# Kernel optimization log

Measured on AMD Instinct MI355X. Metric: run time of the kernel, lower is better.

The kernel has to match this reference:

```python
import jax, jax.numpy as jnp
import numpy as np

B = 16
H = W = 56
C = 384
WS = 7            # window size
SS = 3            # shift size
NH = 12           # num heads
HD = C // NH      # head dim
N = WS * WS       # tokens per window (49)
NW = (H // WS) * (W // WS)  # windows per image (64)
HID = 4 * C       # MLP hidden
SCALE = HD ** -0.5
EPS = 1e-5


def _rel_pos_index():
    coords = np.stack(np.meshgrid(np.arange(WS), np.arange(WS), indexing='ij')).reshape(2, -1)
    rel = (coords[:, :, None] - coords[:, None, :]).transpose(1, 2, 0)  # [N,N,2]
    rel[:, :, 0] += WS - 1
    rel[:, :, 1] += WS - 1
    rel[:, :, 0] *= 2 * WS - 1
    return rel.sum(-1).astype(np.int32)  # [N,N] in [0, (2WS-1)^2)


def _attn_mask():
    img = np.zeros((H, W))
    cnt = 0
    for hs in (slice(0, -WS), slice(-WS, -SS), slice(-SS, None)):
        for ws in (slice(0, -WS), slice(-WS, -SS), slice(-SS, None)):
            img[hs, ws] = cnt
            cnt += 1
    mw = img.reshape(H // WS, WS, W // WS, WS).transpose(0, 2, 1, 3).reshape(-1, N)  # [NW,N]
    d = mw[:, None, :] - mw[:, :, None]  # [NW,N,N]
    return np.where(d != 0, -100.0, 0.0).astype(np.float32)


def setup_inputs() -> dict:
    key = jax.random.key(0)
    ks = jax.random.split(key, 8)
    std = 0.02
    return {
        'x': jax.random.normal(ks[0], (B, H * W, C), jnp.float32),
        'g1': jnp.ones((C,), jnp.float32),
        'b1': jnp.zeros((C,), jnp.float32),
        'qkv_w': jax.random.normal(ks[1], (C, 3 * C), jnp.float32) * std,
        'qkv_b': jnp.zeros((3 * C,), jnp.float32),
        'rpb_table': jax.random.normal(ks[2], ((2 * WS - 1) ** 2, NH), jnp.float32) * std,
        'proj_w': jax.random.normal(ks[3], (C, C), jnp.float32) * std,
        'proj_b': jnp.zeros((C,), jnp.float32),
        'g2': jnp.ones((C,), jnp.float32),
        'b2': jnp.zeros((C,), jnp.float32),
        'fc1_w': jax.random.normal(ks[4], (C, HID), jnp.float32) * std,
        'fc1_b': jnp.zeros((HID,), jnp.float32),
        'fc2_w': jax.random.normal(ks[5], (HID, C), jnp.float32) * std,
        'fc2_b': jnp.zeros((C,), jnp.float32),
        'rel_idx': jnp.asarray(_rel_pos_index()),
        'attn_mask': jnp.asarray(_attn_mask()),
    }


def _ln(x, g, b):
    m = x.mean(-1, keepdims=True)
    v = ((x - m) ** 2).mean(-1, keepdims=True)
    return (x - m) / jnp.sqrt(v + EPS) * g + b


def reference(x, g1, b1, qkv_w, qkv_b, rpb_table, proj_w, proj_b,
              g2, b2, fc1_w, fc1_b, fc2_w, fc2_b, rel_idx, attn_mask):
    shortcut = x
    h = _ln(x, g1, b1).reshape(B, H, W, C)
    # cyclic shift
    h = jnp.roll(h, (-SS, -SS), axis=(1, 2))
    # window partition -> [B*NW, N, C]
    win = h.reshape(B, H // WS, WS, W // WS, WS, C).transpose(0, 1, 3, 2, 4, 5).reshape(-1, N, C)
    # qkv
    qkv = (win @ qkv_w + qkv_b).reshape(-1, N, 3, NH, HD).transpose(2, 0, 3, 1, 4)
    q, k, v = qkv[0] * SCALE, qkv[1], qkv[2]  # [B*NW, NH, N, HD]
    attn = jnp.einsum('bhnd,bhmd->bhnm', q, k)  # [B*NW, NH, N, N]
    # relative position bias
    rpb = rpb_table[rel_idx.reshape(-1)].reshape(N, N, NH).transpose(2, 0, 1)  # [NH,N,N]
    attn = attn + rpb[None]
    # shifted-window attention mask
    attn = attn.reshape(B, NW, NH, N, N) + attn_mask[None, :, None]
    attn = jax.nn.softmax(attn.reshape(-1, NH, N, N), axis=-1)
    out = jnp.einsum('bhnm,bhmd->bhnd', attn, v).transpose(0, 2, 1, 3).reshape(-1, N, C)
    out = out @ proj_w + proj_b
    # window reverse + reverse shift
    out = out.reshape(B, H // WS, W // WS, WS, WS, C).transpose(0, 1, 3, 2, 4, 5).reshape(B, H, W, C)
    out = jnp.roll(out, (SS, SS), axis=(1, 2)).reshape(B, H * W, C)
    x = shortcut + out
    # MLP (exact GELU, as nn.GELU default)
    h2 = _ln(x, g2, b2)
    h2 = jax.nn.gelu(h2 @ fc1_w + fc1_b, approximate=False) @ fc2_w + fc2_b
    return x + h2
```

## Files before the change

### kernel.cpp

```cpp
#include <hip/hip_runtime.h>
#include <hip/hip_bf16.h>
#include <math.h>

typedef __hip_bfloat16 bf16;
typedef __attribute__((ext_vector_type(8))) short short8;
typedef __attribute__((ext_vector_type(4))) float f32x4;

#define C_DIM 384
#define SS 3
#define SCALE_ATTN 0.17677669529663687f
#define LN_EPS 1e-5f

typedef const __attribute__((address_space(1))) void g_cvoid;
typedef __attribute__((address_space(3))) void l_void;
__device__ __forceinline__ void gl_lds16(const void* g, void* l) {
    __builtin_amdgcn_global_load_lds((g_cvoid*)g, (l_void*)l, 16, 0, 0);
}

__global__ void transpose_cast_kernel(const float* __restrict__ in, bf16* __restrict__ out,
                                      int R, int Cc) {
    int idx = blockIdx.x * 256 + threadIdx.x;
    if (idx < R * Cc) {
        int r = idx / Cc, c = idx - r * Cc;
        out[(size_t)c * R + r] = __float2bfloat16(in[idx]);
    }
}

__global__ void build_bm_kernel(const float* __restrict__ rpb, const int* __restrict__ rel_idx,
                                const float* __restrict__ mask, float* __restrict__ BM) {
    int idx = blockIdx.x * 256 + threadIdx.x;
    int col = idx & 63, row = (idx >> 6) & 63;
    int h = (idx >> 12) % 12, wi = idx / (12 * 4096);
    float v = -1e30f;
    if (row < 49 && col < 49)
        v = rpb[rel_idx[row * 49 + col] * 12 + h] + mask[(size_t)wi * 2401 + row * 49 + col];
    BM[idx] = v;
}

__global__ __launch_bounds__(256)
void ln1_shift_window(const float* __restrict__ x, const float* __restrict__ g,
                      const float* __restrict__ bta, bf16* __restrict__ win) {
    int wave = threadIdx.x >> 6, lane = threadIdx.x & 63;
    int token = blockIdx.x * 4 + wave;
    int bw = token / 49, ntk = token - bw * 49;
    int bb = bw >> 6, wi = bw & 63;
    int wh = wi >> 3, wwi = wi & 7;
    int rr = ntk / 7, cc = ntk - rr * 7;
    int hs = wh * 7 + rr + SS; if (hs >= 56) hs -= 56;
    int ws = wwi * 7 + cc + SS; if (ws >= 56) ws -= 56;
    const float* src = x + ((size_t)(bb * 3136 + hs * 56 + ws)) * C_DIM;

    float v[6]; float s = 0.f, sq = 0.f;
    #pragma unroll
    for (int j = 0; j < 6; j++) {
        v[j] = src[lane + j * 64];
        s += v[j]; sq += v[j] * v[j];
    }
    #pragma unroll
    for (int o = 32; o > 0; o >>= 1) { s += __shfl_xor(s, o, 64); sq += __shfl_xor(sq, o, 64); }
    float mean = s * (1.0f / 384.0f);
    float var  = sq * (1.0f / 384.0f) - mean * mean;
    float rstd = rsqrtf(var + LN_EPS);

    bf16* dst = win + (size_t)token * C_DIM;
    #pragma unroll
    for (int j = 0; j < 6; j++) {
        int c = lane + j * 64;
        dst[c] = __float2bfloat16((v[j] - mean) * rstd * g[c] + bta[c]);
    }
}

__global__ __launch_bounds__(256)
void ln2_kernel(const float* __restrict__ xmid, const float* __restrict__ g,
                const float* __restrict__ bta, bf16* __restrict__ out) {
    int wave = threadIdx.x >> 6, lane = threadIdx.x & 63;
    int token = blockIdx.x * 4 + wave;
    const float* src = xmid + (size_t)token * C_DIM;
    float v[6]; float s = 0.f, sq = 0.f;
    #pragma unroll
    for (int j = 0; j < 6; j++) {
        v[j] = src[lane + j * 64];
        s += v[j]; sq += v[j] * v[j];
    }
    #pragma unroll
    for (int o = 32; o > 0; o >>= 1) { s += __shfl_xor(s, o, 64); sq += __shfl_xor(sq, o, 64); }
    float mean = s * (1.0f / 384.0f);
    float var  = sq * (1.0f / 384.0f) - mean * mean;
    float rstd = rsqrtf(var + LN_EPS);
    bf16* dst = out + (size_t)token * C_DIM;
    #pragma unroll
    for (int j = 0; j < 6; j++) {
        int c = lane + j * 64;
        dst[c] = __float2bfloat16((v[j] - mean) * rstd * g[c] + bta[c]);
    }
}

template <int MODE>
__global__ __launch_bounds__(256)
void gemm_kernel(const bf16* __restrict__ A, const bf16* __restrict__ BT,
                 const float* __restrict__ bias, void* __restrict__ out,
                 const float* __restrict__ resid, int M, int N, int K) {
    __shared__ bf16 As[8192];
    __shared__ bf16 Bs[8192];

    int tid = threadIdx.x;
    int wave = tid >> 6, lane = tid & 63, quad = lane >> 4, r = lane & 15;
    int wave_m = wave & 1, wave_n = wave >> 1;
    int m0 = blockIdx.x * 128, n0 = blockIdx.y * 128;

    f32x4 acc[4][4] = {};

    for (int k0 = 0; k0 < K; k0 += 64) {
        #pragma unroll
        for (int c = 0; c < 4; c++) {
            int slot = c * 256 + wave * 64 + lane;
            int panel = slot >> 7, row = slot & 127;
            gl_lds16(A + (size_t)(m0 + row) * K + k0 + panel * 8, &As[(c * 256 + wave * 64) * 8]);
            gl_lds16(BT + (size_t)(n0 + row) * K + k0 + panel * 8, &Bs[(c * 256 + wave * 64) * 8]);
        }
        __syncthreads();

        #pragma unroll
        for (int ks = 0; ks < 2; ks++) {
            int pq = ks * 4 + quad;
            short8 a[4], b[4];
            #pragma unroll
            for (int mt = 0; mt < 4; mt++)
                a[mt] = *(const short8*)&As[(pq * 128 + wave_m * 64 + mt * 16 + r) * 8];
            #pragma unroll
            for (int nt = 0; nt < 4; nt++)
                b[nt] = *(const short8*)&Bs[(pq * 128 + wave_n * 64 + nt * 16 + r) * 8];
            #pragma unroll
            for (int mt = 0; mt < 4; mt++)
                #pragma unroll
                for (int nt = 0; nt < 4; nt++)
                    acc[mt][nt] = __builtin_amdgcn_mfma_f32_16x16x32_bf16(
                        a[mt], b[nt], acc[mt][nt], 0, 0, 0);
        }
        __syncthreads();
    }

    #pragma unroll
    for (int mt = 0; mt < 4; mt++) {
        #pragma unroll
        for (int nt = 0; nt < 4; nt++) {
            int n = n0 + wave_n * 64 + nt * 16 + r;
            float bv = bias[n];
            #pragma unroll
            for (int reg = 0; reg < 4; reg++) {
                int m = m0 + wave_m * 64 + mt * 16 + quad * 4 + reg;
                float v = acc[mt][nt][reg] + bv;
                if (MODE == 0) {
                    ((bf16*)out)[(size_t)m * N + n] = __float2bfloat16(v);
                } else if (MODE == 1) {
                    float gl = 0.5f * v * (1.0f + erff(v * 0.70710678118654752f));
                    ((bf16*)out)[(size_t)m * N + n] = __float2bfloat16(gl);
                } else if (MODE == 2) {
                    int bw = m / 49, ntk = m - bw * 49;
                    int bb = bw >> 6, wi = bw & 63;
                    int wh = wi >> 3, wwi = wi & 7;
                    int rr = ntk / 7, cc = ntk - rr * 7;
                    int ho = wh * 7 + rr + SS; if (ho >= 56) ho -= 56;
                    int wo = wwi * 7 + cc + SS; if (wo >= 56) wo -= 56;
                    size_t dst = ((size_t)(bb * 3136 + ho * 56 + wo)) * C_DIM + n;
                    ((float*)out)[dst] = v + resid[dst];
                } else {
                    size_t idx = (size_t)m * N + n;
                    ((float*)out)[idx] = v + resid[idx];
                }
            }
        }
    }
}

__global__ __launch_bounds__(256)
void attn_mfma_kernel(const bf16* __restrict__ qkv, const float* __restrict__ BM,
                      bf16* __restrict__ out) {
    __shared__ bf16 P_lds[4][4096];
    __shared__ bf16 V_lds[4][2048];
    int wave = threadIdx.x >> 6, lane = threadIdx.x & 63;
    int quad = lane >> 4, m16 = lane & 15;
    int bw = blockIdx.x;
    int h = blockIdx.y * 4 + wave;
    int wi = bw & 63;

    const bf16* base = qkv + (size_t)bw * 49 * 1152 + h * 32;

    bf16* Vt = V_lds[wave];
    #pragma unroll
    for (int it = 0; it < 16; it++) {
        int idx = it * 64 + lane;
        int n = idx >> 4, dp = idx & 15;
        int d0 = dp * 2;
        unsigned val = 0;
        if (n < 49)
            val = *(const unsigned*)(base + (size_t)n * 1152 + 768 + d0);
        bf16 v0 = ((const bf16*)&val)[0], v1 = ((const bf16*)&val)[1];
        int cb = (n & 56);
        Vt[d0 * 64 + ((cb ^ ((d0 & 7) << 3)) | (n & 7))] = v0;
        int d1 = d0 + 1;
        Vt[d1 * 64 + ((cb ^ ((d1 & 7) << 3)) | (n & 7))] = v1;
    }

    short8 qf[4], kf[4];
    #pragma unroll
    for (int t = 0; t < 4; t++) {
        int row = t * 16 + m16;
        int rc = (row < 49) ? row : 0;
        qf[t] = *(const short8*)(base + (size_t)rc * 1152 + quad * 8);
        kf[t] = *(const short8*)(base + (size_t)rc * 1152 + 384 + quad * 8);
    }
    f32x4 S[4][4] = {};
    #pragma unroll
    for (int mt = 0; mt < 4; mt++)
        #pragma unroll
        for (int nt = 0; nt < 4; nt++)
            S[mt][nt] = __builtin_amdgcn_mfma_f32_16x16x32_bf16(qf[mt], kf[nt], S[mt][nt], 0, 0, 0);

    const float* bmw = BM + (((size_t)wi * 12 + h) << 12);
    bf16* Pw = P_lds[wave];
    #pragma unroll
    for (int mt = 0; mt < 4; mt++) {
        #pragma unroll
        for (int reg = 0; reg < 4; reg++) {
            int row = mt * 16 + quad * 4 + reg;
            float p[4];
            float mx = -1e30f;
            #pragma unroll
            for (int nt = 0; nt < 4; nt++) {
                int col = nt * 16 + m16;
                float s = S[mt][nt][reg] * SCALE_ATTN + bmw[row * 64 + col];
                p[nt] = s;
                mx = fmaxf(mx, s);
            }
            #pragma unroll
            for (int o = 1; o < 16; o <<= 1) mx = fmaxf(mx, __shfl_xor(mx, o, 64));
            float sm = 0.f;
            #pragma unroll
            for (int nt = 0; nt < 4; nt++) { p[nt] = __expf(p[nt] - mx); sm += p[nt]; }
            #pragma unroll
            for (int o = 1; o < 16; o <<= 1) sm += __shfl_xor(sm, o, 64);
            float inv = 1.0f / sm;
            int r7 = (row & 7) << 3;
            #pragma unroll
            for (int nt = 0; nt < 4; nt++) {
                int col = nt * 16 + m16;
                int sw = ((col & 56) ^ r7) | (col & 7);
                Pw[row * 64 + sw] = __float2bfloat16(p[nt] * inv);
            }
        }
    }

    f32x4 O[4][2] = {};
    #pragma unroll
    for (int ks = 0; ks < 2; ks++) {
        int chunk = ks * 4 + quad;
        short8 pa[4], vb[2];
        #pragma unroll
        for (int mt = 0; mt < 4; mt++) {
            int row = mt * 16 + m16;
            pa[mt] = *(const short8*)&Pw[row * 64 + ((chunk ^ (row & 7)) << 3)];
        }
        #pragma unroll
        for (int nt = 0; nt < 2; nt++) {
            int d = nt * 16 + m16;
            vb[nt] = *(const short8*)&Vt[d * 64 + ((chunk ^ (d & 7)) << 3)];
        }
        #pragma unroll
        for (int mt = 0; mt < 4; mt++)
            #pragma unroll
            for (int nt = 0; nt < 2; nt++)
                O[mt][nt] = __builtin_amdgcn_mfma_f32_16x16x32_bf16(pa[mt], vb[nt], O[mt][nt], 0, 0, 0);
    }

    bf16* orow = out + (size_t)bw * 49 * 384 + h * 32;
    #pragma unroll
    for (int mt = 0; mt < 4; mt++) {
        #pragma unroll
        for (int reg = 0; reg < 4; reg++) {
            int row = mt * 16 + quad * 4 + reg;
            if (row < 49) {
                #pragma unroll
                for (int nt = 0; nt < 2; nt++)
                    orow[(size_t)row * 384 + nt * 16 + m16] = __float2bfloat16(O[mt][nt][reg]);
            }
        }
    }
}

extern "C" void kernel_launch(void* const* d_in, const int* in_sizes, int n_in,
                              void* d_out, int out_size, void* d_ws, size_t ws_size,
                              hipStream_t stream) {
    const float* x      = (const float*)d_in[0];
    const float* g1     = (const float*)d_in[1];
    const float* b1     = (const float*)d_in[2];
    const float* qkv_w  = (const float*)d_in[3];
    const float* qkv_b  = (const float*)d_in[4];
    const float* rpb    = (const float*)d_in[5];
    const float* proj_w = (const float*)d_in[6];
    const float* proj_b = (const float*)d_in[7];
    const float* g2     = (const float*)d_in[8];
    const float* b2     = (const float*)d_in[9];
    const float* fc1_w  = (const float*)d_in[10];
    const float* fc1_b  = (const float*)d_in[11];
    const float* fc2_w  = (const float*)d_in[12];
    const float* fc2_b  = (const float*)d_in[13];
    const int*   rel_idx   = (const int*)d_in[14];
    const float* attn_mask = (const float*)d_in[15];

    const int M = 50176;

    char* ws = (char*)d_ws;
    size_t off = 0;
    bf16* bufA   = (bf16*)(ws + off); off += (size_t)M * 384 * 2;
    bf16* bufBC  = (bf16*)(ws + off); off += (size_t)M * 1536 * 2;
    float* xmid  = (float*)(ws + off); off += (size_t)M * 384 * 4;
    bf16* qkv_wT  = (bf16*)(ws + off); off += (size_t)1152 * 384 * 2;
    bf16* proj_wT = (bf16*)(ws + off); off += (size_t)384 * 384 * 2;
    bf16* fc1_wT  = (bf16*)(ws + off); off += (size_t)1536 * 384 * 2;
    bf16* fc2_wT  = (bf16*)(ws + off); off += (size_t)384 * 1536 * 2;
    float* BM = (float*)(bufBC + (size_t)M * 1152);

    build_bm_kernel<<<64 * 12 * 4096 / 256, 256, 0, stream>>>(rpb, rel_idx, attn_mask, BM);

    transpose_cast_kernel<<<(384 * 1152 + 255) / 256, 256, 0, stream>>>(qkv_w, qkv_wT, 384, 1152);
    transpose_cast_kernel<<<(384 * 384 + 255) / 256, 256, 0, stream>>>(proj_w, proj_wT, 384, 384);
    transpose_cast_kernel<<<(384 * 1536 + 255) / 256, 256, 0, stream>>>(fc1_w, fc1_wT, 384, 1536);
    transpose_cast_kernel<<<(1536 * 384 + 255) / 256, 256, 0, stream>>>(fc2_w, fc2_wT, 1536, 384);

    ln1_shift_window<<<M / 4, 256, 0, stream>>>(x, g1, b1, bufA);

    gemm_kernel<0><<<dim3(M / 128, 1152 / 128), 256, 0, stream>>>(
        bufA, qkv_wT, qkv_b, bufBC, nullptr, M, 1152, 384);

    attn_mfma_kernel<<<dim3(1024, 3), 256, 0, stream>>>(bufBC, BM, bufA);

    gemm_kernel<2><<<dim3(M / 128, 384 / 128), 256, 0, stream>>>(
        bufA, proj_wT, proj_b, xmid, x, M, 384, 384);

    ln2_kernel<<<M / 4, 256, 0, stream>>>(xmid, g2, b2, bufA);

    gemm_kernel<1><<<dim3(M / 128, 1536 / 128), 256, 0, stream>>>(
        bufA, fc1_wT, fc1_b, bufBC, nullptr, M, 1536, 384);

    gemm_kernel<3><<<dim3(M / 128, 384 / 128), 256, 0, stream>>>(
        bufBC, fc2_wT, fc2_b, d_out, xmid, M, 384, 1536);
}
```

Baseline: 804.6 us.

## Double-buffer GEMM LDS tiles and remap blocks to XCD-contiguous tiles

The GEMM kernel now uses two LDS buffers per operand, so the next K-tile's global-to-LDS load is issued before the current tile's MFMA work and the loop needs one barrier per iteration instead of two. The 2D grid becomes 1D, with block IDs remapped so that consecutive tiles land on the same XCD and share N-tiles of the same M-row in L2. This doubles LDS use to 64 KB per block, which may lower occupancy.

```diff
diff --git a/kernel.cpp b/kernel.cpp
--- a/kernel.cpp
+++ b/kernel.cpp
@@ -100,36 +100,48 @@
 void gemm_kernel(const bf16* __restrict__ A, const bf16* __restrict__ BT,
                  const float* __restrict__ bias, void* __restrict__ out,
                  const float* __restrict__ resid, int M, int N, int K) {
-    __shared__ bf16 As[8192];
-    __shared__ bf16 Bs[8192];
+    __shared__ bf16 As[2][8192];
+    __shared__ bf16 Bs[2][8192];
 
     int tid = threadIdx.x;
     int wave = tid >> 6, lane = tid & 63, quad = lane >> 4, r = lane & 15;
     int wave_m = wave & 1, wave_n = wave >> 1;
-    int m0 = blockIdx.x * 128, n0 = blockIdx.y * 128;
+
+    int nN = N >> 7;
+    int nwg = gridDim.x;
+    int bid = blockIdx.x;
+    int q8 = nwg >> 3, r8 = nwg & 7;
+    int xcd = bid & 7, loc = bid >> 3;
+    int swz = (xcd < r8 ? xcd * (q8 + 1) : r8 * (q8 + 1) + (xcd - r8) * q8) + loc;
+    int mtile = swz / nN;
+    int ntile = swz - mtile * nN;
+    int m0 = mtile << 7, n0 = ntile << 7;
 
     f32x4 acc[4][4] = {};
 
-    for (int k0 = 0; k0 < K; k0 += 64) {
+    auto stage = [&](int buf, int k0) {
         #pragma unroll
         for (int c = 0; c < 4; c++) {
             int slot = c * 256 + wave * 64 + lane;
             int panel = slot >> 7, row = slot & 127;
-            gl_lds16(A + (size_t)(m0 + row) * K + k0 + panel * 8, &As[(c * 256 + wave * 64) * 8]);
-            gl_lds16(BT + (size_t)(n0 + row) * K + k0 + panel * 8, &Bs[(c * 256 + wave * 64) * 8]);
-        }
-        __syncthreads();
-
+            gl_lds16(A + (size_t)(m0 + row) * K + k0 + panel * 8,
+                     &As[buf][(c * 256 + wave * 64) * 8]);
+            gl_lds16(BT + (size_t)(n0 + row) * K + k0 + panel * 8,
+                     &Bs[buf][(c * 256 + wave * 64) * 8]);
+        }
+    };
+
+    auto compute = [&](int buf) {
         #pragma unroll
         for (int ks = 0; ks < 2; ks++) {
             int pq = ks * 4 + quad;
             short8 a[4], b[4];
             #pragma unroll
             for (int mt = 0; mt < 4; mt++)
-                a[mt] = *(const short8*)&As[(pq * 128 + wave_m * 64 + mt * 16 + r) * 8];
+                a[mt] = *(const short8*)&As[buf][(pq * 128 + wave_m * 64 + mt * 16 + r) * 8];
             #pragma unroll
             for (int nt = 0; nt < 4; nt++)
-                b[nt] = *(const short8*)&Bs[(pq * 128 + wave_n * 64 + nt * 16 + r) * 8];
+                b[nt] = *(const short8*)&Bs[buf][(pq * 128 + wave_n * 64 + nt * 16 + r) * 8];
             #pragma unroll
             for (int mt = 0; mt < 4; mt++)
                 #pragma unroll
@@ -137,8 +149,20 @@
                     acc[mt][nt] = __builtin_amdgcn_mfma_f32_16x16x32_bf16(
                         a[mt], b[nt], acc[mt][nt], 0, 0, 0);
         }
+    };
+
+    stage(0, 0);
+    __syncthreads();
+
+    int nk = K >> 6;
+    int cur = 0;
+    for (int kt = 0; kt < nk - 1; kt++) {
+        stage(cur ^ 1, (kt + 1) << 6);
+        compute(cur);
         __syncthreads();
-    }
+        cur ^= 1;
+    }
+    compute(cur);
 
     #pragma unroll
     for (int mt = 0; mt < 4; mt++) {
@@ -330,19 +354,19 @@
 
     ln1_shift_window<<<M / 4, 256, 0, stream>>>(x, g1, b1, bufA);
 
-    gemm_kernel<0><<<dim3(M / 128, 1152 / 128), 256, 0, stream>>>(
+    gemm_kernel<0><<<(M / 128) * (1152 / 128), 256, 0, stream>>>(
         bufA, qkv_wT, qkv_b, bufBC, nullptr, M, 1152, 384);
 
     attn_mfma_kernel<<<dim3(1024, 3), 256, 0, stream>>>(bufBC, BM, bufA);
 
-    gemm_kernel<2><<<dim3(M / 128, 384 / 128), 256, 0, stream>>>(
+    gemm_kernel<2><<<(M / 128) * (384 / 128), 256, 0, stream>>>(
         bufA, proj_wT, proj_b, xmid, x, M, 384, 384);
 
     ln2_kernel<<<M / 4, 256, 0, stream>>>(xmid, g2, b2, bufA);
 
-    gemm_kernel<1><<<dim3(M / 128, 1536 / 128), 256, 0, stream>>>(
+    gemm_kernel<1><<<(M / 128) * (1536 / 128), 256, 0, stream>>>(
         bufA, fc1_wT, fc1_b, bufBC, nullptr, M, 1536, 384);
 
-    gemm_kernel<3><<<dim3(M / 128, 384 / 128), 256, 0, stream>>>(
+    gemm_kernel<3><<<(M / 128) * (384 / 128), 256, 0, stream>>>(
         bufBC, fc2_wT, fc2_b, d_out, xmid, M, 384, 1536);
 }
```

After: 795.2 us. Within noise of the previous version (-1.2%).
